# Kernel optimization log

Hardware: AMD Instinct MI355X
Metric: run time of the kernel (lower is better)

## Reference

```python
import jax, jax.numpy as jnp
import numpy as np

N, M, D = 131072, 32, 32


def setup_inputs() -> dict:
    key = jax.random.key(0)
    k1, k2, k3, k4 = jax.random.split(key, 4)
    # scale points/centers so Mahalanobis distances are O(1) and exp(-d) is well-conditioned
    points = 0.2 * jax.random.normal(k1, (N, D), dtype=jnp.float32)
    centers = 0.2 * jax.random.normal(k2, (M, D), dtype=jnp.float32)
    covs_inv_sqrt = jnp.eye(D, dtype=jnp.float32)[None] + 0.05 * jax.random.normal(k3, (M, D, D), dtype=jnp.float32)
    weights = jax.random.normal(k4, (M,), dtype=jnp.float32)
    return {"points": points, "centers": centers, "covs_inv_sqrt": covs_inv_sqrt, "weights": weights}


def reference(points, centers, covs_inv_sqrt, weights):
    # refresh(): covs_inv = L @ L^T, coefs = softmax(weights) * sqrt(det(covs_inv))
    A = jnp.einsum('mdk,mek->mde', covs_inv_sqrt, covs_inv_sqrt)  # (M, D, D)
    coefs = jax.nn.softmax(weights) * jnp.sqrt(jnp.linalg.det(A))  # (M,)

    # weightedsqdist: d_nm = (x_n - c_m)^T A_m (x_n - c_m), expanded to avoid (N,M,D) diff
    xAx = jnp.einsum('nd,mde,ne->nm', points, A, points)          # (N, M)
    Ac = jnp.einsum('mde,me->md', A, centers)                     # (M, D)
    xAc = jnp.einsum('nd,md->nm', points, Ac)                     # (N, M)
    cAc = jnp.einsum('md,md->m', centers, Ac)                     # (M,)
    dists = xAx - 2.0 * xAc + cAc[None, :]

    # coefs * exp(-dists) with mixture reduction over centers (KeOps sum over j)
    return jnp.exp(-dists) @ coefs  # (N,)
```

## Files before the change

kernel.cpp:

```cpp
#include <hip/hip_runtime.h>
#include <hip/hip_bf16.h>


#define D 32
#define M 32
#define WT 2

typedef __attribute__((ext_vector_type(8))) short short8;
typedef __attribute__((ext_vector_type(4))) float f32x4;

__device__ __forceinline__ unsigned short f2bf_rne(float f) {
  unsigned int u = __float_as_uint(f);
  return (unsigned short)((u + 0x7FFFu + ((u >> 16) & 1u)) >> 16);
}

#define ROR_ADD(x, ctrl) \
  ((x) + __int_as_float(__builtin_amdgcn_mov_dpp(__float_as_int(x), (ctrl), 0xf, 0xf, true)))

__global__ __launch_bounds__(64) void gmm_pre(
    const float* __restrict__ centers, const float* __restrict__ L,
    const float* __restrict__ weights,
    float* __restrict__ C2f, float* __restrict__ coefs,
    unsigned short* __restrict__ LH, unsigned short* __restrict__ LL) {
  __shared__ float U[D][D + 1];
  const int m = blockIdx.x;
  const int t = threadIdx.x;
  const float* Lm = L + m * (D * D);

  if (t < D) {
    for (int k = 0; k < D; ++k) U[t][k] = Lm[t * D + k];
    float acc = 0.f;
    for (int d = 0; d < D; ++d) acc = fmaf(centers[m * D + d], Lm[d * D + t], acc);
    C2f[m * D + t] = acc;
  }

  {
    const int col = t & 15;
    const int dbase = 8 * (t >> 4);
    for (int kt = 0; kt < 2; ++kt) {
      for (int j = 0; j < 8; ++j) {
        const int d = dbase + j;
        const int k = kt * 16 + col;
        float v = Lm[d * D + k];
        unsigned int hi = __float_as_uint(v) & 0xFFFF0000u;
        float lo = v - __uint_as_float(hi);
        size_t off = (((size_t)(m * 2 + kt)) * 64 + t) * 8 + j;
        LH[off] = (unsigned short)(hi >> 16);
        LL[off] = f2bf_rne(lo);
      }
    }
  }
  __syncthreads();

  for (int p = 0; p < D - 1; ++p) {
    if (t > p && t < D) {
      float f = U[t][p] / U[p][p];
      for (int k = p; k < D; ++k) U[t][k] -= f * U[p][k];
    }
    __syncthreads();
  }
  if (t == 0) {
    float det = 1.f;
    for (int i = 0; i < D; ++i) det *= U[i][i];
    float mx = -1e30f;
    for (int j = 0; j < M; ++j) mx = fmaxf(mx, weights[j]);
    float s = 0.f;
    for (int j = 0; j < M; ++j) s += __expf(weights[j] - mx);
    coefs[m] = (__expf(weights[m] - mx) / s) * fabsf(det);
  }
}

__global__ __launch_bounds__(256) void gmm_main(
    const float* __restrict__ points,
    const float* __restrict__ C2f, const float* __restrict__ coefs,
    const unsigned short* __restrict__ LH, const unsigned short* __restrict__ LL,
    float* __restrict__ out, int N) {
  const int lane = threadIdx.x & 63;
  const int wave = threadIdx.x >> 6;
  const int col = lane & 15;
  const int g = lane >> 4;
  const int tileBase = (blockIdx.x * 4 + wave) * (WT * 16);
  if (tileBase >= N) return;

  short8 xh[WT], xl[WT];
#pragma unroll
  for (int t = 0; t < WT; ++t) {
    const float* p = points + (size_t)(tileBase + t * 16 + col) * D + 8 * g;
    float4 a = *reinterpret_cast<const float4*>(p);
    float4 b = *reinterpret_cast<const float4*>(p + 4);
    float v[8] = {a.x, a.y, a.z, a.w, b.x, b.y, b.z, b.w};
    unsigned int hiu[8];
    unsigned int lou[8];
#pragma unroll
    for (int j = 0; j < 8; ++j) {
      unsigned int u = __float_as_uint(v[j]);
      hiu[j] = u & 0xFFFF0000u;
      lou[j] = __float_as_uint(v[j] - __uint_as_float(hiu[j]));
    }
    union { short8 s; unsigned int w[4]; } H, Lo;
#pragma unroll
    for (int jj = 0; jj < 4; ++jj) {
      H.w[jj]  = __builtin_amdgcn_perm(hiu[2 * jj + 1], hiu[2 * jj], 0x07060302);
      Lo.w[jj] = __builtin_amdgcn_perm(lou[2 * jj + 1], lou[2 * jj], 0x07060302);
    }
    xh[t] = H.s;
    xl[t] = Lo.s;
  }

  f32x4 result[WT];
#pragma unroll
  for (int t = 0; t < WT; ++t) result[t] = (f32x4){0.f, 0.f, 0.f, 0.f};

#pragma unroll 2
  for (int m = 0; m < M; ++m) {
    const short8* bhp = reinterpret_cast<const short8*>(LH + (size_t)(m * 2) * 64 * 8);
    const short8* blp = reinterpret_cast<const short8*>(LL + (size_t)(m * 2) * 64 * 8);
    short8 bh0 = bhp[lane];
    short8 bh1 = bhp[64 + lane];
    short8 bl0 = blp[lane];
    short8 bl1 = blp[64 + lane];
    const float c0 = C2f[m * D + col];
    const float c1 = C2f[m * D + 16 + col];
    const float coef = coefs[m];

#pragma unroll
    for (int t = 0; t < WT; ++t) {
      f32x4 acc0 = (f32x4){-c0, -c0, -c0, -c0};
      f32x4 acc1 = (f32x4){-c1, -c1, -c1, -c1};
      acc0 = __builtin_amdgcn_mfma_f32_16x16x32_bf16(xh[t], bh0, acc0, 0, 0, 0);
      acc0 = __builtin_amdgcn_mfma_f32_16x16x32_bf16(xl[t], bh0, acc0, 0, 0, 0);
      acc0 = __builtin_amdgcn_mfma_f32_16x16x32_bf16(xh[t], bl0, acc0, 0, 0, 0);
      acc1 = __builtin_amdgcn_mfma_f32_16x16x32_bf16(xh[t], bh1, acc1, 0, 0, 0);
      acc1 = __builtin_amdgcn_mfma_f32_16x16x32_bf16(xl[t], bh1, acc1, 0, 0, 0);
      acc1 = __builtin_amdgcn_mfma_f32_16x16x32_bf16(xh[t], bl1, acc1, 0, 0, 0);

#pragma unroll
      for (int r = 0; r < 4; ++r) {
        float s = fmaf(acc0[r], acc0[r], acc1[r] * acc1[r]);
        s = ROR_ADD(s, 0x128);
        s = ROR_ADD(s, 0x124);
        s = ROR_ADD(s, 0x122);
        s = ROR_ADD(s, 0x121);
        result[t][r] = fmaf(coef, __expf(-s), result[t][r]);
      }
    }
  }

  if (col == 0) {
#pragma unroll
    for (int t = 0; t < WT; ++t)
#pragma unroll
      for (int r = 0; r < 4; ++r)
        out[tileBase + t * 16 + 4 * g + r] = result[t][r];
  }
}

extern "C" void kernel_launch(void* const* d_in, const int* in_sizes, int n_in,
                              void* d_out, int out_size, void* d_ws, size_t ws_size,
                              hipStream_t stream) {
  const float* points  = (const float*)d_in[0];
  const float* centers = (const float*)d_in[1];
  const float* L       = (const float*)d_in[2];
  const float* weights = (const float*)d_in[3];
  float* out = (float*)d_out;
  const int N = in_sizes[0] / D;

  char* ws = (char*)d_ws;
  float* C2f            = (float*)ws;
  float* coefs          = (float*)(ws + 4096);
  unsigned short* LHf   = (unsigned short*)(ws + 4352);
  unsigned short* LLf   = (unsigned short*)(ws + 4352 + 65536);

  gmm_pre<<<M, 64, 0, stream>>>(centers, L, weights, C2f, coefs, LHf, LLf);

  const int ptsPerBlock = 4 * WT * 16;
  gmm_main<<<(N + ptsPerBlock - 1) / ptsPerBlock, 256, 0, stream>>>(
      points, C2f, coefs, LHf, LLf, out, N);
}
```

Baseline: 122.9 us.

## Transpose-reduce row sums and fold log2 scaling into precomputed factors

The Cholesky factor and centers are pre-scaled by sqrt(log2 e), and coefs are stored as log2, so each exponential becomes a single exp2(lc - v) with no separate multiply. The column reduction is restructured: the four accumulator rows are partially reduced with two DPP steps, each lane then selects one row, and two more DPP steps finish it. This cuts the per-tile work from four full reductions and four exps to four half-reductions plus one exp per lane. The m loop unroll rises to 4. It adds selects and changes rounding slightly through the scaling and the log/exp2 path.

```diff
diff --git a/kernel.cpp b/kernel.cpp
--- a/kernel.cpp
+++ b/kernel.cpp
@@ -14,15 +14,18 @@
   return (unsigned short)((u + 0x7FFFu + ((u >> 16) & 1u)) >> 16);
 }
 
-#define ROR_ADD(x, ctrl) \
+#define DPP_ADD(x, ctrl) \
   ((x) + __int_as_float(__builtin_amdgcn_mov_dpp(__float_as_int(x), (ctrl), 0xf, 0xf, true)))
+
+#define SCL 1.2011224087864498f
 
 __global__ __launch_bounds__(64) void gmm_pre(
     const float* __restrict__ centers, const float* __restrict__ L,
     const float* __restrict__ weights,
-    float* __restrict__ C2f, float* __restrict__ coefs,
+    float2* __restrict__ CN, float* __restrict__ LC,
     unsigned short* __restrict__ LH, unsigned short* __restrict__ LL) {
   __shared__ float U[D][D + 1];
+  __shared__ float C2s[D];
   const int m = blockIdx.x;
   const int t = threadIdx.x;
   const float* Lm = L + m * (D * D);
@@ -31,7 +34,7 @@
     for (int k = 0; k < D; ++k) U[t][k] = Lm[t * D + k];
     float acc = 0.f;
     for (int d = 0; d < D; ++d) acc = fmaf(centers[m * D + d], Lm[d * D + t], acc);
-    C2f[m * D + t] = acc;
+    C2s[t] = acc;
   }
 
   {
@@ -41,7 +44,7 @@
       for (int j = 0; j < 8; ++j) {
         const int d = dbase + j;
         const int k = kt * 16 + col;
-        float v = Lm[d * D + k];
+        float v = Lm[d * D + k] * SCL;
         unsigned int hi = __float_as_uint(v) & 0xFFFF0000u;
         float lo = v - __uint_as_float(hi);
         size_t off = (((size_t)(m * 2 + kt)) * 64 + t) * 8 + j;
@@ -51,6 +54,8 @@
     }
   }
   __syncthreads();
+
+  CN[m * 64 + t] = make_float2(-SCL * C2s[t & 15], -SCL * C2s[16 + (t & 15)]);
 
   for (int p = 0; p < D - 1; ++p) {
     if (t > p && t < D) {
@@ -66,13 +71,14 @@
     for (int j = 0; j < M; ++j) mx = fmaxf(mx, weights[j]);
     float s = 0.f;
     for (int j = 0; j < M; ++j) s += __expf(weights[j] - mx);
-    coefs[m] = (__expf(weights[m] - mx) / s) * fabsf(det);
+    float coef = (__expf(weights[m] - mx) / s) * fabsf(det);
+    LC[m] = log2f(coef);
   }
 }
 
 __global__ __launch_bounds__(256) void gmm_main(
     const float* __restrict__ points,
-    const float* __restrict__ C2f, const float* __restrict__ coefs,
+    const float2* __restrict__ CN, const float* __restrict__ LC,
     const unsigned short* __restrict__ LH, const unsigned short* __restrict__ LL,
     float* __restrict__ out, int N) {
   const int lane = threadIdx.x & 63;
@@ -81,6 +87,9 @@
   const int g = lane >> 4;
   const int tileBase = (blockIdx.x * 4 + wave) * (WT * 16);
   if (tileBase >= N) return;
+
+  const bool b0 = (lane >> 2) & 1;
+  const bool b1 = (lane >> 2) & 2;
 
   short8 xh[WT], xl[WT];
 #pragma unroll
@@ -107,26 +116,26 @@
     xl[t] = Lo.s;
   }
 
-  f32x4 result[WT];
+  float result[WT];
 #pragma unroll
-  for (int t = 0; t < WT; ++t) result[t] = (f32x4){0.f, 0.f, 0.f, 0.f};
+  for (int t = 0; t < WT; ++t) result[t] = 0.f;
 
-#pragma unroll 2
+  const short8* bh_base = reinterpret_cast<const short8*>(LH);
+  const short8* bl_base = reinterpret_cast<const short8*>(LL);
+
+#pragma unroll 4
   for (int m = 0; m < M; ++m) {
-    const short8* bhp = reinterpret_cast<const short8*>(LH + (size_t)(m * 2) * 64 * 8);
-    const short8* blp = reinterpret_cast<const short8*>(LL + (size_t)(m * 2) * 64 * 8);
-    short8 bh0 = bhp[lane];
-    short8 bh1 = bhp[64 + lane];
-    short8 bl0 = blp[lane];
-    short8 bl1 = blp[64 + lane];
-    const float c0 = C2f[m * D + col];
-    const float c1 = C2f[m * D + 16 + col];
-    const float coef = coefs[m];
+    short8 bh0 = bh_base[(m * 2 + 0) * 64 + lane];
+    short8 bh1 = bh_base[(m * 2 + 1) * 64 + lane];
+    short8 bl0 = bl_base[(m * 2 + 0) * 64 + lane];
+    short8 bl1 = bl_base[(m * 2 + 1) * 64 + lane];
+    const float2 cn = CN[m * 64 + lane];
+    const float lc = LC[m];
 
 #pragma unroll
     for (int t = 0; t < WT; ++t) {
-      f32x4 acc0 = (f32x4){-c0, -c0, -c0, -c0};
-      f32x4 acc1 = (f32x4){-c1, -c1, -c1, -c1};
+      f32x4 acc0 = (f32x4){cn.x, cn.x, cn.x, cn.x};
+      f32x4 acc1 = (f32x4){cn.y, cn.y, cn.y, cn.y};
       acc0 = __builtin_amdgcn_mfma_f32_16x16x32_bf16(xh[t], bh0, acc0, 0, 0, 0);
       acc0 = __builtin_amdgcn_mfma_f32_16x16x32_bf16(xl[t], bh0, acc0, 0, 0, 0);
       acc0 = __builtin_amdgcn_mfma_f32_16x16x32_bf16(xh[t], bl0, acc0, 0, 0, 0);
@@ -134,24 +143,30 @@
       acc1 = __builtin_amdgcn_mfma_f32_16x16x32_bf16(xl[t], bh1, acc1, 0, 0, 0);
       acc1 = __builtin_amdgcn_mfma_f32_16x16x32_bf16(xh[t], bl1, acc1, 0, 0, 0);
 
-#pragma unroll
-      for (int r = 0; r < 4; ++r) {
-        float s = fmaf(acc0[r], acc0[r], acc1[r] * acc1[r]);
-        s = ROR_ADD(s, 0x128);
-        s = ROR_ADD(s, 0x124);
-        s = ROR_ADD(s, 0x122);
-        s = ROR_ADD(s, 0x121);
-        result[t][r] = fmaf(coef, __expf(-s), result[t][r]);
+      float sq0, sq1, sq2, sq3;
+      {
+        float s0 = fmaf(acc0[0], acc0[0], acc1[0] * acc1[0]);
+        float s1 = fmaf(acc0[1], acc0[1], acc1[1] * acc1[1]);
+        float s2 = fmaf(acc0[2], acc0[2], acc1[2] * acc1[2]);
+        float s3 = fmaf(acc0[3], acc0[3], acc1[3] * acc1[3]);
+        s0 = DPP_ADD(s0, 0x128); s0 = DPP_ADD(s0, 0x124);
+        s1 = DPP_ADD(s1, 0x128); s1 = DPP_ADD(s1, 0x124);
+        s2 = DPP_ADD(s2, 0x128); s2 = DPP_ADD(s2, 0x124);
+        s3 = DPP_ADD(s3, 0x128); s3 = DPP_ADD(s3, 0x124);
+        sq0 = s0; sq1 = s1; sq2 = s2; sq3 = s3;
       }
+      float v = b1 ? (b0 ? sq3 : sq2) : (b0 ? sq1 : sq0);
+      v = DPP_ADD(v, 0xB1);
+      v = DPP_ADD(v, 0x4E);
+      result[t] += exp2f(lc - v);
     }
   }
 
-  if (col == 0) {
+  if ((lane & 3) == 0) {
+    const int q = (lane >> 2) & 3;
 #pragma unroll
     for (int t = 0; t < WT; ++t)
-#pragma unroll
-      for (int r = 0; r < 4; ++r)
-        out[tileBase + t * 16 + 4 * g + r] = result[t][r];
+      out[tileBase + t * 16 + 4 * g + q] = result[t];
   }
 }
 
@@ -166,14 +181,14 @@
   const int N = in_sizes[0] / D;
 
   char* ws = (char*)d_ws;
-  float* C2f            = (float*)ws;
-  float* coefs          = (float*)(ws + 4096);
-  unsigned short* LHf   = (unsigned short*)(ws + 4352);
-  unsigned short* LLf   = (unsigned short*)(ws + 4352 + 65536);
+  float2* CN          = (float2*)ws;
+  float* LC           = (float*)(ws + 16384);
+  unsigned short* LHf = (unsigned short*)(ws + 32768);
+  unsigned short* LLf = (unsigned short*)(ws + 98304);
 
-  gmm_pre<<<M, 64, 0, stream>>>(centers, L, weights, C2f, coefs, LHf, LLf);
+  gmm_pre<<<M, 64, 0, stream>>>(centers, L, weights, CN, LC, LHf, LLf);
 
   const int ptsPerBlock = 4 * WT * 16;
   gmm_main<<<(N + ptsPerBlock - 1) / ptsPerBlock, 256, 0, stream>>>(
-      points, C2f, coefs, LHf, LLf, out, N);
+      points, CN, LC, LHf, LLf, out, N);
 }
```

Result: no change. 122.1 us (-0.7%).
